# Kernel tuning notes

Measured on AMD Instinct MI355X. Metric: run time of the kernel, lower is better.

The kernel has to match this reference:

```python
import jax, jax.numpy as jnp
import numpy as np

EMBED_K = 64
DISEN_K = [4, 4]           # channels per layer
WEIGHT_SIZE_LIST = [64, 64, 64]
TEMPERATURE = 1.0
ROUTING_ITERATIONS = 3
N_LAYERS = 2
EPS = 1e-12


def setup_inputs() -> dict:
    key = jax.random.key(0)
    ks = jax.random.split(key, 8)
    num_users, num_items = 500000, 200000
    n_neigh = 4096
    params = {}
    for layer in range(N_LAYERS):
        k_ch = DISEN_K[layer]
        d_in = WEIGHT_SIZE_LIST[layer]
        d_out = WEIGHT_SIZE_LIST[layer + 1] // k_ch
        params[f"W{layer}"] = jax.random.normal(ks[4 + layer], (k_ch, d_in, d_out), dtype=jnp.float32) * 0.1
        params[f"b{layer}"] = jnp.zeros((k_ch, d_out), dtype=jnp.float32)
    return {
        "user": 123,
        "item": 77,
        "neigh_user": jax.random.randint(ks[0], (n_neigh,), 0, num_items),   # item ids
        "neigh_item": jax.random.randint(ks[1], (n_neigh,), 0, num_users),   # user ids
        "Gu": jax.random.normal(ks[2], (num_users, EMBED_K), dtype=jnp.float32) * 0.1,
        "Gi": jax.random.normal(ks[3], (num_items, EMBED_K), dtype=jnp.float32) * 0.1,
        **params,
    }


def _project(x, W, b):
    # FeatureProjection: per-channel linear + relu. x: [N, d_in] -> [N, K, d_out]
    return jax.nn.relu(jnp.einsum('ni,kid->nkd', x, W) + b)


def _route_once(z):
    # One DisenGCNLayer call on star graph: node 0 = ego, nodes 1..N = neighbors.
    # L2-normalize per channel (torch F.normalize p=2, dim=-1)
    nrm = jnp.maximum(jnp.linalg.norm(z, axis=-1, keepdims=True), EPS)
    zn = z / nrm                              # [N+1, K, d]
    ego = zn[0]                               # [K, d]
    nb = zn[1:]                               # [N, K, d]
    # routing probs: softmax over channels K of similarity / temperature
    p = jax.nn.softmax(jnp.einsum('nkd,kd->nk', nb, ego) / TEMPERATURE, axis=-1)
    # aggregated ego capsule per channel
    return jnp.einsum('nk,nkd->kd', p, nb)    # [K, d]


def _forward(Gu, Gi, W0, b0, W1, b1, user, item, neigh_user, neigh_item):
    # ego user + its item neighbors; ego item + its user neighbors
    eu = jnp.concatenate([Gu[user][None, :], Gi[neigh_user]], axis=0)   # [N+1, 64]
    ei = jnp.concatenate([Gi[item][None, :], Gu[neigh_item]], axis=0)   # [N+1, 64]
    for (W, b) in ((W0, b0), (W1, b1)):
        zu = _project(eu, W, b)               # [N+1, K, d]
        zi = _project(ei, W, b)
        for _ in range(ROUTING_ITERATIONS):
            zu = zu.at[0].set(_route_once(zu))
            zi = zi.at[0].set(_route_once(zi))
        eu = zu.reshape(zu.shape[0], -1)      # [N+1, K*d]
        ei = zi.reshape(zi.shape[0], -1)
        # message dropout = 0.0 -> identity
    xui = jnp.sum(eu[0] * ei[0])[None]        # shape (1,)
    return xui, eu[0], ei[0]


def reference(user, item, neigh_user, neigh_item, Gu, Gi, W0, b0, W1, b1):
    return _forward(Gu, Gi, W0, b0, W1, b1, user, item, neigh_user, neigh_item)
```

## Files before the change

kernel.cpp:

```cpp
#include <hip/hip_runtime.h>
#include <hip/hip_bf16.h>


#define EPS 1e-12f
#define LOG2E 1.44269504088896f
#define SPB 8
#define NBK (2 * SPB)

__device__ __forceinline__ float g16sum(float v) {
    v += __shfl_xor(v, 1, 64);
    v += __shfl_xor(v, 2, 64);
    v += __shfl_xor(v, 4, 64);
    v += __shfl_xor(v, 8, 64);
    return v;
}
__device__ __forceinline__ unsigned short f2bf(float f) {
    unsigned int b = __float_as_uint(f);
    b += 0x7fffu + ((b >> 16) & 1u);
    return (unsigned short)(b >> 16);
}
__device__ __forceinline__ float bf2f(unsigned short u) {
    return __uint_as_float(((unsigned int)u) << 16);
}
__device__ __forceinline__ float bflo(unsigned int w) {
    return __uint_as_float(w << 16);
}
__device__ __forceinline__ float bfhi(unsigned int w) {
    return __uint_as_float(w & 0xffff0000u);
}

__device__ __forceinline__ unsigned long long pack2(float f0, float f1,
                                                    unsigned int gen16) {
    const unsigned long long a = __float_as_uint(f0) >> 8;
    const unsigned long long b = __float_as_uint(f1) >> 8;
    return (a << 40) | (b << 16) | (unsigned long long)gen16;
}
__device__ __forceinline__ float unpack0(unsigned long long v) {
    return __uint_as_float((unsigned int)(v >> 40) << 8);
}
__device__ __forceinline__ float unpack1(unsigned long long v) {
    return __uint_as_float(((unsigned int)(v >> 16) & 0xffffffu) << 8);
}
__device__ __forceinline__ unsigned long long slot_poll(unsigned long long* p,
                                                        unsigned int gen16) {
    unsigned long long v;
    for (;;) {
        v = atomicAdd(p, 0ull);
        if ((unsigned int)(v & 0xffffull) == gen16) break;
        __builtin_amdgcn_s_sleep(1);
    }
    return v;
}

__device__ __forceinline__ float proj_row4(const float xa[4],
                                           const float* __restrict__ W,
                                           const float* __restrict__ b, int lane) {
    const int k = lane >> 4, d = lane & 15;
    float sum = b[k * 16 + d];
    const float* __restrict__ Wp = W + k * 1024 + d;
#pragma unroll
    for (int i = 0; i < 64; ++i)
        sum = fmaf(__shfl(xa[i & 3], i >> 2, 64), Wp[i * 16], sum);
    return fmaxf(sum, 0.f);
}

__global__ __launch_bounds__(256) void k1_gather_proj2(
    const int* __restrict__ user, const int* __restrict__ item,
    const int* __restrict__ nu, const int* __restrict__ ni,
    const float* __restrict__ Gu, const float* __restrict__ Gi,
    const float* __restrict__ W0, const float* __restrict__ b0,
    const float* __restrict__ W1, const float* __restrict__ b1,
    unsigned short* __restrict__ znbA, unsigned short* __restrict__ znbB,
    unsigned int* __restrict__ call_ctr, int n_rows)
{
    if (blockIdx.x == 0 && threadIdx.x == 0) atomicAdd(call_ctr, 1u);

    const int lane = threadIdx.x & 63;
    const int wv   = threadIdx.x >> 6;
    const int rr   = blockIdx.x * 4 + wv;
    if (rr >= 2 * n_rows) return;
    const int side = rr >= n_rows;
    const int n    = rr - side * n_rows;
    const int c    = lane & 15;

    int idx; const float* G;
    if (n == 0) { idx = side ? item[0] : user[0];     G = side ? Gi : Gu; }
    else        { idx = side ? ni[n - 1] : nu[n - 1]; G = side ? Gu : Gi; }
    const float4 xv = ((const float4*)(G + (size_t)idx * 64))[c];
    const float xa[4] = {xv.x, xv.y, xv.z, xv.w};

    const float z0 = proj_row4(xa, W0, b0, lane);
    const float nrm0 = fmaxf(sqrtf(g16sum(z0 * z0)), EPS);
    znbA[(size_t)rr * 64 + lane] = f2bf(z0 / nrm0);

    if (n == 0) return;

    float xa2[4];
#pragma unroll
    for (int jj = 0; jj < 4; ++jj) xa2[jj] = __shfl(z0, (c << 2) | jj, 64);
    const float z1 = proj_row4(xa2, W1, b1, lane);
    const float nrm1 = fmaxf(sqrtf(g16sum(z1 * z1)), EPS);
    znbB[(size_t)rr * 64 + lane] = f2bf(z1 / nrm1);
}

__global__ __launch_bounds__(1024) void k2_route_all(
    const unsigned short* __restrict__ znbA, const unsigned short* __restrict__ znbB,
    const float* __restrict__ W1, const float* __restrict__ b1,
    unsigned long long* __restrict__ slots,
    const unsigned int* __restrict__ call_ctr,
    float* __restrict__ out, int n_neigh)
{
    const int n_rows = n_neigh + 1;
    const int tid  = threadIdx.x;
    const int lane = tid & 63;
    const int wv   = tid >> 6;
    const int side = blockIdx.x & 1;
    const int bg   = blockIdx.x >> 1;
    const unsigned short* __restrict__ zA = znbA + (size_t)side * n_rows * 64;
    const unsigned short* __restrict__ zB = znbB + (size_t)side * n_rows * 64;
    const unsigned int genbase = (*call_ctr) * 8u;

    __shared__ float sW[4096];
    __shared__ float red[16][64];
    __shared__ float sEgo[64];
    __shared__ float sTmp[64];

    for (int q = tid; q < 4096; q += 1024) {
        const int i = q >> 6, m = q & 63;
        sW[q] = W1[(m >> 4) * 1024 + i * 16 + (m & 15)];
    }
    if (tid < 64) sEgo[tid] = bf2f(zA[tid]) * LOG2E;
    __syncthreads();

    const int j   = lane & 7;
    const int rg0 = bg * 128 + (tid >> 3);

    for (int s = 0; s < 6; ++s) {
        const unsigned short* __restrict__ zb = (s < 3) ? zA : zB;
        const unsigned int gen = (genbase + (unsigned int)s + 1u) & 0xffffu;
        float ego[8];
#pragma unroll
        for (int m = 0; m < 8; ++m) ego[m] = sEgo[j * 8 + m];

        float a8[8] = {0.f, 0.f, 0.f, 0.f, 0.f, 0.f, 0.f, 0.f};
        for (int r = rg0; r < n_neigh; r += SPB * 128) {
            const uint4 q = *(const uint4*)(zb + (((size_t)r + 1) << 6) + (j << 3));
            float x[8];
            x[0] = bflo(q.x); x[1] = bfhi(q.x);
            x[2] = bflo(q.y); x[3] = bfhi(q.y);
            x[4] = bflo(q.z); x[5] = bfhi(q.z);
            x[6] = bflo(q.w); x[7] = bfhi(q.w);
            float partial = 0.f;
#pragma unroll
            for (int m = 0; m < 8; ++m) partial = fmaf(x[m], ego[m], partial);
            const float dp = partial + __shfl_xor(partial, 1, 64);
            const float eo = exp2f(dp);
            float den = eo + __shfl_xor(eo, 2, 64);
            den += __shfl_xor(den, 4, 64);
            const float p = eo * __builtin_amdgcn_rcpf(den);
#pragma unroll
            for (int m = 0; m < 8; ++m) a8[m] = fmaf(p, x[m], a8[m]);
        }
#pragma unroll
        for (int mask = 8; mask <= 32; mask <<= 1)
#pragma unroll
            for (int m = 0; m < 8; ++m) a8[m] += __shfl_xor(a8[m], mask, 64);
        if (lane < 8) {
#pragma unroll
            for (int m = 0; m < 8; ++m) red[wv][lane * 8 + m] = a8[m];
        }
        __syncthreads();

        unsigned long long* slotbase = slots + (size_t)(s * 2 + side) * SPB * 32;
        if (wv == 0) {
            float ssum = 0.f;
#pragma unroll
            for (int w = 0; w < 16; ++w) ssum += red[w][lane];
            const float f0 = __shfl(ssum, (lane & 31) * 2, 64);
            const float f1 = __shfl(ssum, (lane & 31) * 2 + 1, 64);
            if (lane < 32)
                atomicExch(&slotbase[bg * 32 + lane], pack2(f0, f1, gen));
        }
        __syncthreads();

        if (s < 5) {
            if (wv < 4) {
                const int p = 2 * wv + (lane >> 5);
                const int e = lane & 31;
                const unsigned long long v = slot_poll(&slotbase[p * 32 + e], gen);
                ((float2*)red[p])[e] = make_float2(unpack0(v), unpack1(v));
            }
            __syncthreads();
            if (wv == 0) {
                float e = 0.f;
#pragma unroll
                for (int bb = 0; bb < SPB; ++bb) e += red[bb][lane];
                if (s == 2) sTmp[lane] = e;
                else sEgo[lane] = (e / fmaxf(sqrtf(g16sum(e * e)), EPS)) * LOG2E;
            }
            __syncthreads();
            if (s == 2) {
                if (wv == 0) {
                    float xa[4];
#pragma unroll
                    for (int jj = 0; jj < 4; ++jj) xa[jj] = sTmp[((lane & 15) << 2) | jj];
                    float sum = b1[lane];
#pragma unroll
                    for (int i = 0; i < 64; ++i)
                        sum = fmaf(__shfl(xa[i & 3], i >> 2, 64), sW[i * 64 + lane], sum);
                    sum = fmaxf(sum, 0.f);
                    sEgo[lane] = (sum / fmaxf(sqrtf(g16sum(sum * sum)), EPS)) * LOG2E;
                }
                __syncthreads();
            }
        } else if (side == 0 && bg == 0) {
            const int g  = wv * 64 + lane;
            const int s2 = g >> 8;
            const int pp = (g >> 5) & 7;
            const int e  = g & 31;
            unsigned long long* sb2 = slots + (size_t)(5 * 2 + s2) * SPB * 32;
            if (wv < 8) {
                const unsigned long long v = slot_poll(&sb2[pp * 32 + e], gen);
                ((float2*)red[s2 * 8 + pp])[e] = make_float2(unpack0(v), unpack1(v));
            }
            __syncthreads();
            if (wv == 0) {
                float u = 0.f, v = 0.f;
#pragma unroll
                for (int w = 0; w < 8; ++w)  u += red[w][lane];
#pragma unroll
                for (int w = 8; w < 16; ++w) v += red[w][lane];
                out[1 + lane]  = u;
                out[65 + lane] = v;
                float p = u * v;
#pragma unroll
                for (int sh = 32; sh >= 1; sh >>= 1) p += __shfl_xor(p, sh, 64);
                if (lane == 0) out[0] = p;
            }
        }
    }
}

extern "C" void kernel_launch(void* const* d_in, const int* in_sizes, int n_in,
                              void* d_out, int out_size, void* d_ws, size_t ws_size,
                              hipStream_t stream) {
    const int*   user       = (const int*)d_in[0];
    const int*   item       = (const int*)d_in[1];
    const int*   neigh_user = (const int*)d_in[2];
    const int*   neigh_item = (const int*)d_in[3];
    const float* Gu         = (const float*)d_in[4];
    const float* Gi         = (const float*)d_in[5];
    const float* W0         = (const float*)d_in[6];
    const float* b0         = (const float*)d_in[7];
    const float* W1         = (const float*)d_in[8];
    const float* b1         = (const float*)d_in[9];
    float* out = (float*)d_out;

    const int n_neigh = in_sizes[2];
    const int n_rows  = n_neigh + 1;
    const size_t rowsz = (size_t)2 * n_rows * 64;

    unsigned short*     znbA  = (unsigned short*)d_ws;
    unsigned short*     znbB  = znbA + rowsz;
    unsigned long long* slots = (unsigned long long*)(znbB + rowsz);
    unsigned int*       ctr   = (unsigned int*)(slots + 6 * 2 * SPB * 32);

    hipLaunchKernelGGL(k1_gather_proj2, dim3((2 * n_rows + 3) / 4), dim3(256), 0, stream,
                       user, item, neigh_user, neigh_item, Gu, Gi, W0, b0, W1, b1,
                       znbA, znbB, ctr, n_rows);
    hipLaunchKernelGGL(k2_route_all, dim3(NBK), dim3(1024), 0, stream,
                       znbA, znbB, W1, b1, slots, ctr, out, n_neigh);
}
```

Before: 46.24 us.

## Move layer-1 projection into routing kernel, overlapping it with cross-block slot waits

```diff
diff --git a/kernel.cpp b/kernel.cpp
--- a/kernel.cpp
+++ b/kernel.cpp
@@ -4,7 +4,7 @@
 
 #define EPS 1e-12f
 #define LOG2E 1.44269504088896f
-#define SPB 8
+#define SPB 16
 #define NBK (2 * SPB)
 
 __device__ __forceinline__ float g16sum(float v) {
@@ -52,9 +52,9 @@
     return v;
 }
 
-__device__ __forceinline__ float proj_row4(const float xa[4],
-                                           const float* __restrict__ W,
-                                           const float* __restrict__ b, int lane) {
+__device__ __forceinline__ float proj_row4_g(const float xa[4],
+                                             const float* __restrict__ W,
+                                             const float* __restrict__ b, int lane) {
     const int k = lane >> 4, d = lane & 15;
     float sum = b[k * 16 + d];
     const float* __restrict__ Wp = W + k * 1024 + d;
@@ -63,14 +63,22 @@
         sum = fmaf(__shfl(xa[i & 3], i >> 2, 64), Wp[i * 16], sum);
     return fmaxf(sum, 0.f);
 }
-
-__global__ __launch_bounds__(256) void k1_gather_proj2(
+__device__ __forceinline__ float proj_row4_l(const float xa[4],
+                                             const float* __restrict__ sW,
+                                             const float* __restrict__ b, int lane) {
+    float sum = b[lane];
+#pragma unroll
+    for (int i = 0; i < 64; ++i)
+        sum = fmaf(__shfl(xa[i & 3], i >> 2, 64), sW[i * 64 + lane], sum);
+    return fmaxf(sum, 0.f);
+}
+
+__global__ __launch_bounds__(256) void k1_gather_proj(
     const int* __restrict__ user, const int* __restrict__ item,
     const int* __restrict__ nu, const int* __restrict__ ni,
     const float* __restrict__ Gu, const float* __restrict__ Gi,
     const float* __restrict__ W0, const float* __restrict__ b0,
-    const float* __restrict__ W1, const float* __restrict__ b1,
-    unsigned short* __restrict__ znbA, unsigned short* __restrict__ znbB,
+    unsigned short* __restrict__ znbA, unsigned short* __restrict__ z0raw,
     unsigned int* __restrict__ call_ctr, int n_rows)
 {
     if (blockIdx.x == 0 && threadIdx.x == 0) atomicAdd(call_ctr, 1u);
@@ -89,22 +97,14 @@
     const float4 xv = ((const float4*)(G + (size_t)idx * 64))[c];
     const float xa[4] = {xv.x, xv.y, xv.z, xv.w};
 
-    const float z0 = proj_row4(xa, W0, b0, lane);
+    const float z0 = proj_row4_g(xa, W0, b0, lane);
     const float nrm0 = fmaxf(sqrtf(g16sum(z0 * z0)), EPS);
     znbA[(size_t)rr * 64 + lane] = f2bf(z0 / nrm0);
-
-    if (n == 0) return;
-
-    float xa2[4];
-#pragma unroll
-    for (int jj = 0; jj < 4; ++jj) xa2[jj] = __shfl(z0, (c << 2) | jj, 64);
-    const float z1 = proj_row4(xa2, W1, b1, lane);
-    const float nrm1 = fmaxf(sqrtf(g16sum(z1 * z1)), EPS);
-    znbB[(size_t)rr * 64 + lane] = f2bf(z1 / nrm1);
+    if (n > 0) z0raw[(size_t)rr * 64 + lane] = f2bf(z0);
 }
 
 __global__ __launch_bounds__(1024) void k2_route_all(
-    const unsigned short* __restrict__ znbA, const unsigned short* __restrict__ znbB,
+    const unsigned short* __restrict__ znbA, const unsigned short* __restrict__ z0raw,
     const float* __restrict__ W1, const float* __restrict__ b1,
     unsigned long long* __restrict__ slots,
     const unsigned int* __restrict__ call_ctr,
@@ -116,14 +116,15 @@
     const int wv   = tid >> 6;
     const int side = blockIdx.x & 1;
     const int bg   = blockIdx.x >> 1;
-    const unsigned short* __restrict__ zA = znbA + (size_t)side * n_rows * 64;
-    const unsigned short* __restrict__ zB = znbB + (size_t)side * n_rows * 64;
+    const unsigned short* __restrict__ zA  = znbA  + (size_t)side * n_rows * 64;
+    const unsigned short* __restrict__ z0r = z0raw + (size_t)side * n_rows * 64;
     const unsigned int genbase = (*call_ctr) * 8u;
 
     __shared__ float sW[4096];
     __shared__ float red[16][64];
     __shared__ float sEgo[64];
     __shared__ float sTmp[64];
+    __shared__ unsigned short zB[256 * 64];
 
     for (int q = tid; q < 4096; q += 1024) {
         const int i = q >> 6, m = q & 63;
@@ -133,18 +134,22 @@
     __syncthreads();
 
     const int j   = lane & 7;
-    const int rg0 = bg * 128 + (tid >> 3);
+    const int g   = tid >> 3;
 
     for (int s = 0; s < 6; ++s) {
-        const unsigned short* __restrict__ zb = (s < 3) ? zA : zB;
         const unsigned int gen = (genbase + (unsigned int)s + 1u) & 0xffffu;
         float ego[8];
 #pragma unroll
         for (int m = 0; m < 8; ++m) ego[m] = sEgo[j * 8 + m];
 
         float a8[8] = {0.f, 0.f, 0.f, 0.f, 0.f, 0.f, 0.f, 0.f};
-        for (int r = rg0; r < n_neigh; r += SPB * 128) {
-            const uint4 q = *(const uint4*)(zb + (((size_t)r + 1) << 6) + (j << 3));
+#pragma unroll
+        for (int m = 0; m < 2; ++m) {
+            const int r = bg * 128 + g + m * (SPB * 128);
+            if (r >= n_neigh) break;
+            uint4 q;
+            if (s < 3) q = *(const uint4*)(zA + (((size_t)r + 1) << 6) + (j << 3));
+            else       q = *(const uint4*)(zB + ((m * 128 + g) << 6) + (j << 3));
             float x[8];
             x[0] = bflo(q.x); x[1] = bfhi(q.x);
             x[2] = bflo(q.y); x[3] = bfhi(q.y);
@@ -152,14 +157,14 @@
             x[6] = bflo(q.w); x[7] = bfhi(q.w);
             float partial = 0.f;
 #pragma unroll
-            for (int m = 0; m < 8; ++m) partial = fmaf(x[m], ego[m], partial);
+            for (int mm = 0; mm < 8; ++mm) partial = fmaf(x[mm], ego[mm], partial);
             const float dp = partial + __shfl_xor(partial, 1, 64);
             const float eo = exp2f(dp);
             float den = eo + __shfl_xor(eo, 2, 64);
             den += __shfl_xor(den, 4, 64);
             const float p = eo * __builtin_amdgcn_rcpf(den);
 #pragma unroll
-            for (int m = 0; m < 8; ++m) a8[m] = fmaf(p, x[m], a8[m]);
+            for (int mm = 0; mm < 8; ++mm) a8[mm] = fmaf(p, x[mm], a8[mm]);
         }
 #pragma unroll
         for (int mask = 8; mask <= 32; mask <<= 1)
@@ -183,8 +188,22 @@
         }
         __syncthreads();
 
+        if (s < 3) {
+            const int lo = s * 86, hi = (s == 2) ? 256 : (s + 1) * 86;
+            for (int L = lo + wv; L < hi; L += 16) {
+                const int r = bg * 128 + (L & 127) + (L >> 7) * (SPB * 128);
+                if (r >= n_neigh) continue;
+                const int c = lane & 15;
+                const ushort4 uv = ((const ushort4*)(z0r + (((size_t)r + 1) << 6)))[c];
+                const float xa[4] = {bf2f(uv.x), bf2f(uv.y), bf2f(uv.z), bf2f(uv.w)};
+                const float z1 = proj_row4_l(xa, sW, b1, lane);
+                const float nrm = fmaxf(sqrtf(g16sum(z1 * z1)), EPS);
+                zB[(L << 6) + lane] = f2bf(z1 / nrm);
+            }
+        }
+
         if (s < 5) {
-            if (wv < 4) {
+            if (wv < 8) {
                 const int p = 2 * wv + (lane >> 5);
                 const int e = lane & 31;
                 const unsigned long long v = slot_poll(&slotbase[p * 32 + e], gen);
@@ -204,35 +223,31 @@
                     float xa[4];
 #pragma unroll
                     for (int jj = 0; jj < 4; ++jj) xa[jj] = sTmp[((lane & 15) << 2) | jj];
-                    float sum = b1[lane];
-#pragma unroll
-                    for (int i = 0; i < 64; ++i)
-                        sum = fmaf(__shfl(xa[i & 3], i >> 2, 64), sW[i * 64 + lane], sum);
-                    sum = fmaxf(sum, 0.f);
+                    const float sum = proj_row4_l(xa, sW, b1, lane);
                     sEgo[lane] = (sum / fmaxf(sqrtf(g16sum(sum * sum)), EPS)) * LOG2E;
                 }
                 __syncthreads();
             }
         } else if (side == 0 && bg == 0) {
-            const int g  = wv * 64 + lane;
-            const int s2 = g >> 8;
-            const int pp = (g >> 5) & 7;
-            const int e  = g & 31;
+            const int P  = 2 * wv + (lane >> 5);
+            const int s2 = P >> 4, bb = P & 15;
+            const int e  = lane & 31;
             unsigned long long* sb2 = slots + (size_t)(5 * 2 + s2) * SPB * 32;
-            if (wv < 8) {
-                const unsigned long long v = slot_poll(&sb2[pp * 32 + e], gen);
-                ((float2*)red[s2 * 8 + pp])[e] = make_float2(unpack0(v), unpack1(v));
-            }
+            const unsigned long long v = slot_poll(&sb2[bb * 32 + e], gen);
+            float f0 = unpack0(v), f1 = unpack1(v);
+            f0 += __shfl_xor(f0, 32, 64);
+            f1 += __shfl_xor(f1, 32, 64);
+            if (lane < 32) ((float2*)red[wv])[e] = make_float2(f0, f1);
             __syncthreads();
             if (wv == 0) {
-                float u = 0.f, v = 0.f;
-#pragma unroll
-                for (int w = 0; w < 8; ++w)  u += red[w][lane];
-#pragma unroll
-                for (int w = 8; w < 16; ++w) v += red[w][lane];
+                float u = 0.f, v2 = 0.f;
+#pragma unroll
+                for (int w = 0; w < 8; ++w)  u  += red[w][lane];
+#pragma unroll
+                for (int w = 8; w < 16; ++w) v2 += red[w][lane];
                 out[1 + lane]  = u;
-                out[65 + lane] = v;
-                float p = u * v;
+                out[65 + lane] = v2;
+                float p = u * v2;
 #pragma unroll
                 for (int sh = 32; sh >= 1; sh >>= 1) p += __shfl_xor(p, sh, 64);
                 if (lane == 0) out[0] = p;
@@ -261,13 +276,13 @@
     const size_t rowsz = (size_t)2 * n_rows * 64;
 
     unsigned short*     znbA  = (unsigned short*)d_ws;
-    unsigned short*     znbB  = znbA + rowsz;
-    unsigned long long* slots = (unsigned long long*)(znbB + rowsz);
+    unsigned short*     z0raw = znbA + rowsz;
+    unsigned long long* slots = (unsigned long long*)(z0raw + rowsz);
     unsigned int*       ctr   = (unsigned int*)(slots + 6 * 2 * SPB * 32);
 
-    hipLaunchKernelGGL(k1_gather_proj2, dim3((2 * n_rows + 3) / 4), dim3(256), 0, stream,
-                       user, item, neigh_user, neigh_item, Gu, Gi, W0, b0, W1, b1,
-                       znbA, znbB, ctr, n_rows);
+    hipLaunchKernelGGL(k1_gather_proj, dim3((2 * n_rows + 3) / 4), dim3(256), 0, stream,
+                       user, item, neigh_user, neigh_item, Gu, Gi, W0, b0,
+                       znbA, z0raw, ctr, n_rows);
     hipLaunchKernelGGL(k2_route_all, dim3(NBK), dim3(1024), 0, stream,
-                       znbA, znbB, W1, b1, slots, ctr, out, n_neigh);
-}
+                       znbA, z0raw, W1, b1, slots, ctr, out, n_neigh);
+}
```

Result: slower. 95.34 us (+106.2%).
